# Optimization experiments

Measured on AMD Instinct MI355X. Metric: run time of the kernel, lower is better.

The kernel has to match this reference:

```python
import jax, jax.numpy as jnp
import numpy as np

B, T, TRAIN = 4, 2048, 1536
D, H, L, FF, V = 512, 8, 12, 2048, 100
DH = D // H
ROPE_BASE = 100000.0


def layer_norm(x, g, b, eps=1e-5):
    mu = jnp.mean(x, axis=-1, keepdims=True)
    var = jnp.mean(jnp.square(x - mu), axis=-1, keepdims=True)
    return (x - mu) * jax.lax.rsqrt(var + eps) * g + b


def rope_cos_sin(t, dh):
    inv_freq = 1.0 / (ROPE_BASE ** (jnp.arange(0, dh, 2, dtype=jnp.float32) / dh))  # (dh/2,)
    ang = jnp.arange(t, dtype=jnp.float32)[:, None] * inv_freq[None, :]  # (T, dh/2)
    return jnp.cos(ang), jnp.sin(ang)


def apply_rope_interleaved(x, cos, sin):
    # x: (B, T, H, DH); interleaved pairs (x0,x1),(x2,x3),...
    x1, x2 = x[..., 0::2], x[..., 1::2]
    c, s = cos[None, :, None, :], sin[None, :, None, :]
    r1 = x1 * c - x2 * s
    r2 = x1 * s + x2 * c
    return jnp.stack([r1, r2], axis=-1).reshape(x.shape)


def setup_inputs() -> dict:
    key = jax.random.key(0)
    ks = jax.random.split(key, 20)
    sc = 0.02
    inp = {
        'R': jax.random.normal(ks[0], (B, T, D), jnp.float32),
        'y_train': jax.random.randint(ks[1], (B, TRAIN), 0, V),
        'emb': jax.random.normal(ks[2], (V, D), jnp.float32) * sc,
        'Wqkv': jax.random.normal(ks[3], (L, D, 3 * D), jnp.float32) * sc,
        'bqkv': jnp.zeros((L, 3 * D), jnp.float32),
        'Wo': jax.random.normal(ks[4], (L, D, D), jnp.float32) * sc,
        'bo': jnp.zeros((L, D), jnp.float32),
        'ln1_g': jnp.ones((L, D), jnp.float32),
        'ln1_b': jnp.zeros((L, D), jnp.float32),
        'ln2_g': jnp.ones((L, D), jnp.float32),
        'ln2_b': jnp.zeros((L, D), jnp.float32),
        'W1': jax.random.normal(ks[5], (L, D, FF), jnp.float32) * sc,
        'b1': jnp.zeros((L, FF), jnp.float32),
        'W2': jax.random.normal(ks[6], (L, FF, D), jnp.float32) * sc,
        'b2': jnp.zeros((L, D), jnp.float32),
        'pW1': jax.random.normal(ks[7], (D, 2 * D), jnp.float32) * sc,
        'pb1': jnp.zeros((2 * D,), jnp.float32),
        'pW2': jax.random.normal(ks[8], (2 * D, V), jnp.float32) * sc,
        'pb2': jnp.zeros((V,), jnp.float32),
    }
    return inp


def icl_forward(R, y_train, emb, Wqkv, bqkv, Wo, bo, ln1_g, ln1_b, ln2_g, ln2_b, W1, b1, W2, b2, pW1, pb1, pW2, pb2):
    b, t, d = R.shape
    train = y_train.shape[1]
    # label embedding: train rows get emb[y], test rows get zeros
    y_emb = jnp.concatenate([emb[y_train], jnp.zeros((b, t - train, d), R.dtype)], axis=1)
    rep = R + y_emb
    # ICL mask: column j visible iff j < train or j == i
    idx = jnp.arange(t)
    allowed = (idx[None, :] < train) | (idx[:, None] == idx[None, :])
    mask = jnp.where(allowed, 0.0, -jnp.inf).astype(R.dtype)  # (T, T)
    cos, sin = rope_cos_sin(t, DH)
    scale = 1.0 / jnp.sqrt(jnp.asarray(DH, R.dtype))

    def block(x, p):
        wqkv, bq, wo, bob, g1, be1, g2, be2, w1, bb1, w2, bb2 = p
        h = layer_norm(x, g1, be1)
        qkv = h @ wqkv + bq  # (B,T,3D)
        q, k, v = jnp.split(qkv, 3, axis=-1)
        q = q.reshape(b, t, H, DH)
        k = k.reshape(b, t, H, DH)
        v = v.reshape(b, t, H, DH)
        q = apply_rope_interleaved(q, cos, sin)
        k = apply_rope_interleaved(k, cos, sin)
        scores = jnp.einsum('bthd,bshd->bhts', q, k) * scale + mask
        attn = jax.nn.softmax(scores, axis=-1)
        o = jnp.einsum('bhts,bshd->bthd', attn, v).reshape(b, t, d)
        x = x + o @ wo + bob
        h2 = layer_norm(x, g2, be2)
        x = x + jax.nn.gelu(h2 @ w1 + bb1) @ w2 + bb2
        return x, None

    rep, _ = jax.lax.scan(block, rep, (Wqkv, bqkv, Wo, bo, ln1_g, ln1_b, ln2_g, ln2_b, W1, b1, W2, b2))
    test = rep[:, train:, :]
    logits = jax.nn.gelu(test @ pW1 + pb1) @ pW2 + pb2  # (B, test, V)
    return logits


def reference(R, y_train, emb, Wqkv, bqkv, Wo, bo, ln1_g, ln1_b, ln2_g, ln2_b, W1, b1, W2, b2, pW1, pb1, pW2, pb2):
    return icl_forward(R, y_train, emb, Wqkv, bqkv, Wo, bo, ln1_g, ln1_b, ln2_g, ln2_b, W1, b1, W2, b2, pW1, pb1, pW2, pb2)
```

## Files before the change

kernel.cpp:

```cpp
#include <hip/hip_runtime.h>
#include <hip/hip_bf16.h>

#define BB 4
#define TT 2048
#define TRAIN 1536
#define DD 512
#define HH 8
#define LL 12
#define FFD 2048
#define VV 100
#define DH 64
#define NT (BB*TT)
#define NTEST (BB*(TT-TRAIN))

typedef __bf16 bf16x8 __attribute__((ext_vector_type(8)));
typedef float  f32x4  __attribute__((ext_vector_type(4)));
typedef unsigned int u32x4 __attribute__((ext_vector_type(4)));

#define GLDS16(g, l) __builtin_amdgcn_global_load_lds( \
    (const __attribute__((address_space(1))) void*)(g), \
    (__attribute__((address_space(3))) void*)(l), 16, 0, 0)

__global__ __launch_bounds__(256) void emb_add(const float* __restrict__ R,
                                               const int* __restrict__ y,
                                               const float* __restrict__ emb,
                                               float* __restrict__ rep) {
    int idx = blockIdx.x * 256 + threadIdx.x;
    int d = idx & 511;
    int n = idx >> 9;
    int t = n & (TT - 1);
    int b = n >> 11;
    float val = R[idx];
    if (t < TRAIN) {
        int tok = y[b * TRAIN + t];
        val += emb[(size_t)tok * DD + d];
    }
    rep[idx] = val;
}

__global__ __launch_bounds__(256) void ln_wave(const float* __restrict__ x,
                                               const float* __restrict__ g,
                                               const float* __restrict__ bta,
                                               __bf16* __restrict__ out) {
    int row = blockIdx.x * 4 + (threadIdx.x >> 6);
    int lane = threadIdx.x & 63;
    const float* xr = x + (size_t)row * DD + lane * 8;
    float4 a = *(const float4*)xr;
    float4 c = *(const float4*)(xr + 4);
    float s  = a.x + a.y + a.z + a.w + c.x + c.y + c.z + c.w;
    float sq = a.x*a.x + a.y*a.y + a.z*a.z + a.w*a.w + c.x*c.x + c.y*c.y + c.z*c.z + c.w*c.w;
#pragma unroll
    for (int off = 1; off < 64; off <<= 1) {
        s  += __shfl_xor(s, off);
        sq += __shfl_xor(sq, off);
    }
    float mu  = s * (1.0f / DD);
    float var = sq * (1.0f / DD) - mu * mu;
    float inv = rsqrtf(var + 1e-5f);
    const float* gp = g + lane * 8;
    const float* bp = bta + lane * 8;
    float4 g0 = *(const float4*)gp, g1 = *(const float4*)(gp + 4);
    float4 b0 = *(const float4*)bp, b1 = *(const float4*)(bp + 4);
    __bf16 o8[8];
    o8[0] = (__bf16)((a.x - mu) * inv * g0.x + b0.x);
    o8[1] = (__bf16)((a.y - mu) * inv * g0.y + b0.y);
    o8[2] = (__bf16)((a.z - mu) * inv * g0.z + b0.z);
    o8[3] = (__bf16)((a.w - mu) * inv * g0.w + b0.w);
    o8[4] = (__bf16)((c.x - mu) * inv * g1.x + b1.x);
    o8[5] = (__bf16)((c.y - mu) * inv * g1.y + b1.y);
    o8[6] = (__bf16)((c.z - mu) * inv * g1.z + b1.z);
    o8[7] = (__bf16)((c.w - mu) * inv * g1.w + b1.w);
    *(uint4*)(out + (size_t)row * DD + lane * 8) = *(uint4*)o8;
}

__global__ __launch_bounds__(256) void rope_tab(float* __restrict__ ctab, float* __restrict__ stab) {
    int idx = blockIdx.x * 256 + threadIdx.x;
    int p = idx & 31, t = idx >> 5;
    double freq = exp(-((double)(2 * p) / 64.0) * log(100000.0));
    double ang = (double)t * freq;
    ctab[idx] = (float)cos(ang);
    stab[idx] = (float)sin(ang);
}

#define QSCALE 0.1803368801111244f
__global__ __launch_bounds__(256) void rope_vt(const __bf16* __restrict__ qkv,
                                               const float* __restrict__ ctab,
                                               const float* __restrict__ stab,
                                               __bf16* __restrict__ qo,
                                               __bf16* __restrict__ ko,
                                               __bf16* __restrict__ vt) {
    int bh = blockIdx.y; int b = bh >> 3, h = bh & 7;
    int t0 = blockIdx.x * 64;
    __shared__ __bf16 tile[64][72];
    int tid = threadIdx.x;
    {
        int r = tid >> 2, cg = (tid & 3) * 16;
        const __bf16* src = qkv + (size_t)(b * TT + t0 + r) * (3 * DD) + 2 * DD + h * DH + cg;
        *(uint4*)&tile[r][cg]     = *(const uint4*)&src[0];
        *(uint4*)&tile[r][cg + 8] = *(const uint4*)&src[8];
    }
#pragma unroll
    for (int c = 0; c < 2; ++c) {
        int lin = c * 256 + tid;
        int tl = lin >> 3, u = lin & 7;
        int t = t0 + tl;
        const __bf16* base = qkv + (size_t)(b * TT + t) * (3 * DD) + h * DH + u * 8;
        uint4 qu = *(const uint4*)base;
        uint4 ku = *(const uint4*)(base + DD);
        float4 cv = *(const float4*)(ctab + t * 32 + u * 4);
        float4 sv = *(const float4*)(stab + t * 32 + u * 4);
        const __bf16* qp = (const __bf16*)&qu;
        const __bf16* kp = (const __bf16*)&ku;
        float cc[4] = {cv.x, cv.y, cv.z, cv.w};
        float ss[4] = {sv.x, sv.y, sv.z, sv.w};
        __bf16 oq[8], ok8[8];
#pragma unroll
        for (int j = 0; j < 4; ++j) {
            float x1 = (float)qp[2 * j], x2 = (float)qp[2 * j + 1];
            float k1 = (float)kp[2 * j], k2 = (float)kp[2 * j + 1];
            oq[2 * j]     = (__bf16)((x1 * cc[j] - x2 * ss[j]) * QSCALE);
            oq[2 * j + 1] = (__bf16)((x1 * ss[j] + x2 * cc[j]) * QSCALE);
            ok8[2 * j]     = (__bf16)(k1 * cc[j] - k2 * ss[j]);
            ok8[2 * j + 1] = (__bf16)(k1 * ss[j] + k2 * cc[j]);
        }
        size_t ob = ((size_t)bh * TT + t) * DH + u * 8;
        *(uint4*)(qo + ob) = *(uint4*)oq;
        *(uint4*)(ko + ob) = *(uint4*)ok8;
    }
    __syncthreads();
    {
        int dh = tid >> 2, tg = (tid & 3) * 16;
        __bf16 outv[16];
#pragma unroll
        for (int j = 0; j < 16; ++j) outv[j] = tile[tg + j][dh];
        __bf16* dst = vt + ((size_t)bh * DH + dh) * TT + t0 + tg;
        *(uint4*)&dst[0] = *(uint4*)&outv[0];
        *(uint4*)&dst[8] = *(uint4*)&outv[8];
    }
}

#define NCH (TRAIN/128)
#define EXP2(d, s) asm("v_exp_f32 %0, %1" : "=v"(d) : "v"(s))

__global__ __launch_bounds__(256, 2) void attn_mfma(const __bf16* __restrict__ q,
                                                    const __bf16* __restrict__ k,
                                                    const __bf16* __restrict__ vt,
                                                    __bf16* __restrict__ obuf) {
    __shared__ __align__(16) __bf16 Kb[2][128 * 64];
    __shared__ __align__(16) __bf16 Vb[2][64 * 128];
    __shared__ float sself[128];

    const int tid = threadIdx.x;
    const int lin = blockIdx.x;
    const int xcd = lin & 7, sblk = lin >> 3;
    const int bh = xcd * 4 + (sblk & 3);
    const int t0q = (sblk >> 2) * 128;
    const int b = bh >> 3, hh = bh & 7;
    const size_t kbase = (size_t)bh * TT * DH;
    const int w = tid >> 6;
    const int lane = tid & 63;
    const int l16 = lane & 15;
    const int quad = lane >> 4;
    const int x7 = l16 & 7;

    bf16x8 qa[2][2];
#pragma unroll
    for (int mi = 0; mi < 2; ++mi)
#pragma unroll
        for (int ks = 0; ks < 2; ++ks) {
            const __bf16* qg = q + kbase + (size_t)(t0q + w * 32 + mi * 16 + l16) * DH + ks * 32 + quad * 8;
            qa[mi][ks] = *(const bf16x8*)qg;
        }

    const int krl = lane >> 3, ksl = lane & 7;
    const int vrl = lane >> 4, vsl = lane & 15;

    f32x4 oa[2][4] = {};
    float lsum[2] = {0.f, 0.f};

    {
#pragma unroll
        for (int c = 0; c < 4; ++c) {
            int rb = w * 4 + c;
            GLDS16(k + kbase + (size_t)(rb * 8 + krl) * DH + ((ksl ^ krl) * 8), &Kb[0][rb * 512]);
            int dh = rb * 4 + vrl;
            GLDS16(vt + kbase + (size_t)dh * TT + ((vsl ^ (dh & 7)) * 8), &Vb[0][rb * 512]);
        }
    }

    for (int ci = 0; ci < NCH; ++ci) {
        __syncthreads();
        if (ci + 1 < NCH) {
            const __bf16* gk = k + kbase + (size_t)((ci + 1) * 128) * DH;
            __bf16* dK = Kb[(ci + 1) & 1];
            __bf16* dV = Vb[(ci + 1) & 1];
#pragma unroll
            for (int c = 0; c < 4; ++c) {
                int rb = w * 4 + c;
                GLDS16(gk + (size_t)(rb * 8 + krl) * DH + ((ksl ^ krl) * 8), dK + rb * 512);
                int dh = rb * 4 + vrl;
                GLDS16(vt + kbase + (size_t)dh * TT + (ci + 1) * 128 + ((vsl ^ (dh & 7)) * 8), dV + rb * 512);
            }
        }

        const __bf16* kc = Kb[ci & 1];
        f32x4 acc[2][8] = {};
        __builtin_amdgcn_s_setprio(1);
#pragma unroll
        for (int ks = 0; ks < 2; ++ks) {
            bf16x8 kf[8];
#pragma unroll
            for (int ni = 0; ni < 8; ++ni)
                kf[ni] = *(const bf16x8*)&kc[(ni * 16 + l16) * 64 + (((ks * 4 + quad) ^ x7) * 8)];
#pragma unroll
            for (int ni = 0; ni < 8; ++ni) {
                acc[0][ni] = __builtin_amdgcn_mfma_f32_16x16x32_bf16(kf[ni], qa[0][ks], acc[0][ni], 0, 0, 0);
                acc[1][ni] = __builtin_amdgcn_mfma_f32_16x16x32_bf16(kf[ni], qa[1][ks], acc[1][ni], 0, 0, 0);
            }
        }
        __builtin_amdgcn_s_setprio(0);

        u32x4 pa[2][4];
#pragma unroll
        for (int mi = 0; mi < 2; ++mi) {
            unsigned int pk[8][2];
            float rs = 0.f;
#pragma unroll
            for (int ni = 0; ni < 8; ++ni) {
                float p0, p1, p2, p3;
                EXP2(p0, acc[mi][ni][0]);
                EXP2(p1, acc[mi][ni][1]);
                EXP2(p2, acc[mi][ni][2]);
                EXP2(p3, acc[mi][ni][3]);
                rs += (p0 + p1) + (p2 + p3);
                asm("v_cvt_pk_bf16_f32 %0, %1, %2" : "=v"(pk[ni][0]) : "v"(p0), "v"(p1));
                asm("v_cvt_pk_bf16_f32 %0, %1, %2" : "=v"(pk[ni][1]) : "v"(p2), "v"(p3));
            }
            rs += __shfl_xor(rs, 16);
            rs += __shfl_xor(rs, 32);
            lsum[mi] += rs;
#pragma unroll
            for (int ks = 0; ks < 4; ++ks)
#pragma unroll
                for (int rr = 0; rr < 2; ++rr) {
                    unsigned int A = pk[2 * ks][rr], Bv = pk[2 * ks + 1][rr];
                    asm("v_permlane32_swap_b32 %0, %1" : "+v"(A), "+v"(Bv));
                    asm("v_permlane16_swap_b32 %0, %1" : "+v"(A), "+v"(Bv));
                    pa[mi][ks][rr]     = A;
                    pa[mi][ks][rr + 2] = Bv;
                }
        }

        const __bf16* vc = Vb[ci & 1];
        __builtin_amdgcn_s_setprio(1);
#pragma unroll
        for (int ks = 0; ks < 4; ++ks) {
            bf16x8 vf[4];
#pragma unroll
            for (int ni = 0; ni < 4; ++ni)
                vf[ni] = *(const bf16x8*)&vc[(ni * 16 + l16) * 128 + (((ks * 4 + quad) ^ x7) * 8)];
            bf16x8 pa0, pa1;
            { u32x4 t = pa[0][ks]; __builtin_memcpy(&pa0, &t, 16); }
            { u32x4 t = pa[1][ks]; __builtin_memcpy(&pa1, &t, 16); }
#pragma unroll
            for (int ni = 0; ni < 4; ++ni) {
                oa[0][ni] = __builtin_amdgcn_mfma_f32_16x16x32_bf16(pa0, vf[ni], oa[0][ni], 0, 0, 0);
                oa[1][ni] = __builtin_amdgcn_mfma_f32_16x16x32_bf16(pa1, vf[ni], oa[1][ni], 0, 0, 0);
            }
        }
        __builtin_amdgcn_s_setprio(0);
    }

    float lr[2][4];
#pragma unroll
    for (int mi = 0; mi < 2; ++mi)
#pragma unroll
        for (int r = 0; r < 4; ++r)
            lr[mi][r] = __shfl(lsum[mi], quad * 4 + r);

    if (t0q >= TRAIN) {
        __syncthreads();
        {
            int dh = tid >> 2, cg = (tid & 3) * 32;
            const __bf16* vg = vt + kbase + (size_t)dh * TT + t0q + cg;
#pragma unroll
            for (int u = 0; u < 4; ++u)
                *(uint4*)&Vb[0][dh * 128 + cg + u * 8] = *(const uint4*)&vg[u * 8];
            int row = tid >> 1, hf = tid & 1;
            const __bf16* qp = q + kbase + (size_t)(t0q + row) * DH + hf * 32;
            const __bf16* kp = k + kbase + (size_t)(t0q + row) * DH + hf * 32;
            float dacc = 0.f;
#pragma unroll
            for (int u = 0; u < 4; ++u) {
                uint4 uq = *(const uint4*)&qp[u * 8];
                uint4 uk = *(const uint4*)&kp[u * 8];
                const __bf16* pq = (const __bf16*)&uq;
                const __bf16* pk2 = (const __bf16*)&uk;
#pragma unroll
                for (int j = 0; j < 8; ++j) dacc += (float)pq[j] * (float)pk2[j];
            }
            dacc += __shfl_xor(dacc, 1);
            sself[row] = dacc;
        }
        __syncthreads();
#pragma unroll
        for (int mi = 0; mi < 2; ++mi)
#pragma unroll
            for (int r = 0; r < 4; ++r) {
                int qr = w * 32 + mi * 16 + quad * 4 + r;
                float pp;
                EXP2(pp, sself[qr]);
                lr[mi][r] += pp;
#pragma unroll
                for (int ni = 0; ni < 4; ++ni)
                    oa[mi][ni][r] += pp * (float)Vb[0][(ni * 16 + l16) * 128 + qr];
            }
    }

#pragma unroll
    for (int mi = 0; mi < 2; ++mi)
#pragma unroll
        for (int r = 0; r < 4; ++r) {
            float inv = 1.f / lr[mi][r];
            int trow = t0q + w * 32 + mi * 16 + quad * 4 + r;
            __bf16* op = obuf + ((size_t)(b * TT) + trow) * DD + hh * 64;
#pragma unroll
            for (int ni = 0; ni < 4; ++ni)
                op[ni * 16 + l16] = (__bf16)(oa[mi][ni][r] * inv);
        }
}

__global__ __launch_bounds__(256) void transpose_pad(const float* __restrict__ src,
                                                     __bf16* __restrict__ dst,
                                                     int K, int N) {
    __shared__ __bf16 t[32][33];
    int n0 = blockIdx.x * 32, k0 = blockIdx.y * 32;
    int tx = threadIdx.x & 31, ty = threadIdx.x >> 5;
#pragma unroll
    for (int i = 0; i < 4; ++i) {
        int nn = n0 + tx;
        t[ty + i * 8][tx] = (nn < N) ? (__bf16)src[(size_t)(k0 + ty + i * 8) * N + nn] : (__bf16)0.f;
    }
    __syncthreads();
#pragma unroll
    for (int i = 0; i < 4; ++i) {
        dst[(size_t)(n0 + ty + i * 8) * K + k0 + tx] = t[tx][ty + i * 8];
    }
}

__global__ __launch_bounds__(256) void transpose_all(const float* __restrict__ s0,
                                                     const float* __restrict__ s1,
                                                     const float* __restrict__ s2,
                                                     const float* __restrict__ s3,
                                                     __bf16* __restrict__ d0, __bf16* __restrict__ d1,
                                                     __bf16* __restrict__ d2, __bf16* __restrict__ d3) {
    int i = blockIdx.x;
    const float* src; __bf16* dst; int K, N, tx, ty;
    if (i < 768)       { src = s0; dst = d0; K = 512;  N = 1536; int j = i;        tx = j % 48; ty = j / 48; }
    else if (i < 1024) { src = s1; dst = d1; K = 512;  N = 512;  int j = i - 768;  tx = j % 16; ty = j / 16; }
    else if (i < 2048) { src = s2; dst = d2; K = 512;  N = 2048; int j = i - 1024; tx = j % 64; ty = j / 64; }
    else               { src = s3; dst = d3; K = 2048; N = 512;  int j = i - 2048; tx = j % 16; ty = j / 16; }
    __shared__ __bf16 t[32][33];
    int n0 = tx * 32, k0 = ty * 32;
    int lx = threadIdx.x & 31, ly = threadIdx.x >> 5;
#pragma unroll
    for (int c = 0; c < 4; ++c)
        t[ly + c * 8][lx] = (__bf16)src[(size_t)(k0 + ly + c * 8) * N + n0 + lx];
    __syncthreads();
#pragma unroll
    for (int c = 0; c < 4; ++c)
        dst[(size_t)(n0 + ly + c * 8) * K + k0 + lx] = t[lx][ly + c * 8];
}

template <int EP, int TN>
__global__ __launch_bounds__(256) void gemm_bt(const __bf16* __restrict__ A,
                                               const __bf16* __restrict__ Bt,
                                               const float* __restrict__ bias,
                                               float* __restrict__ resid,
                                               __bf16* __restrict__ Cout,
                                               int M, int N, int K) {
    constexpr int NI = TN / 32;
    __shared__ __align__(16) __bf16 As[2][128 * 32];
    __shared__ __align__(16) __bf16 Bs[2][TN * 32];
    const int tid = threadIdx.x;
    const int gx = gridDim.x;
    const int linb = blockIdx.x + gx * blockIdx.y;
    const int xs = gx >> 3;
    const int xcd = linb & 7, sb = linb >> 3;
    const int bx = xcd * xs + (sb % xs);
    const int by = sb / xs;
    const int m0 = bx * 128;
    const int n0 = by * TN;
    const int lane = tid & 63;
    const int w = tid >> 6;
    const int wm = (w >> 1) * 64, wn = (w & 1) * (TN / 2);
    const int lrow = lane & 15;
    const int kq = (lane >> 4) * 8;

    f32x4 acc[4][NI] = {};

    const int srA = w * 32 + (lane >> 2);
    const int srB = w * (TN / 4) + (lane >> 2);
    const int scol = (lane & 3) * 8;
    const __bf16* gA = A  + (size_t)(m0 + srA) * K + scol;
    const __bf16* gB = Bt + (size_t)(n0 + srB) * K + scol;
    __bf16* lA0 = &As[0][(w * 32) * 32];
    __bf16* lA0b = lA0 + 16 * 32;
    __bf16* lA1 = &As[1][(w * 32) * 32];
    __bf16* lA1b = lA1 + 16 * 32;
    __bf16* lB0 = &Bs[0][(w * (TN / 4)) * 32];
    __bf16* lB1 = &Bs[1][(w * (TN / 4)) * 32];

    const int nk = K >> 6;
    for (int kt = 0; kt < nk; ++kt) {
        const int k0 = kt << 6;
        GLDS16(gA + k0,            lA0);
        GLDS16(gA + 16 * K + k0,   lA0b);
        GLDS16(gA + k0 + 32,       lA1);
        GLDS16(gA + 16 * K + k0 + 32, lA1b);
        GLDS16(gB + k0,            lB0);
        GLDS16(gB + k0 + 32,       lB1);
        if constexpr (TN == 128) {
            GLDS16(gB + 16 * K + k0,      lB0 + 16 * 32);
            GLDS16(gB + 16 * K + k0 + 32, lB1 + 16 * 32);
        }
        __syncthreads();
#pragma unroll
        for (int ps = 0; ps < 2; ++ps) {
            bf16x8 afr[4], bfr[NI];
#pragma unroll
            for (int i = 0; i < 4; ++i)
                afr[i] = *(const bf16x8*)&As[ps][(wm + i * 16 + lrow) * 32 + kq];
#pragma unroll
            for (int i = 0; i < NI; ++i)
                bfr[i] = *(const bf16x8*)&Bs[ps][(wn + i * 16 + lrow) * 32 + kq];
#pragma unroll
            for (int mi = 0; mi < 4; ++mi)
#pragma unroll
                for (int ni = 0; ni < NI; ++ni)
                    acc[mi][ni] = __builtin_amdgcn_mfma_f32_16x16x32_bf16(afr[mi], bfr[ni], acc[mi][ni], 0, 0, 0);
        }
        __syncthreads();
    }

    const int crow = (lane >> 4) * 4;
    const int ccol = lane & 15;
#pragma unroll
    for (int mi = 0; mi < 4; ++mi) {
#pragma unroll
        for (int ni = 0; ni < NI; ++ni) {
            int gn = n0 + wn + ni * 16 + ccol;
            float bv = bias[gn];
#pragma unroll
            for (int r = 0; r < 4; ++r) {
                int gm = m0 + wm + mi * 16 + crow + r;
                float vvv = acc[mi][ni][r] + bv;
                if constexpr (EP == 1) {
                    float x = vvv;
                    vvv = x / (1.f + __expf(-1.5957691216f * (x + 0.044715f * x * x * x)));
                }
                if constexpr (EP == 2) {
                    resid[(size_t)gm * N + gn] += vvv;
                } else if constexpr (EP == 4) {
                    if (gn < VV) resid[(size_t)gm * VV + gn] = vvv;
                } else {
                    Cout[(size_t)gm * N + gn] = (__bf16)vvv;
                }
            }
        }
    }
}

__global__ __launch_bounds__(256) void cast_test(const float* __restrict__ rep, __bf16* __restrict__ testb) {
    int idx = blockIdx.x * 256 + threadIdx.x;
    int d = idx & 511;
    int i = idx >> 9;
    int ttk = i & 511;
    int b = i >> 9;
    testb[idx] = (__bf16)rep[(size_t)(b * TT + TRAIN + ttk) * DD + d];
}

__global__ void pad_bias(const float* __restrict__ pb2, float* __restrict__ pb2p) {
    int t = threadIdx.x;
    if (t < 128) pb2p[t] = (t < VV) ? pb2[t] : 0.f;
}

extern "C" void kernel_launch(void* const* d_in, const int* in_sizes, int n_in,
                              void* d_out, int out_size, void* d_ws, size_t ws_size,
                              hipStream_t stream) {
    const float* R    = (const float*)d_in[0];
    const int*   y    = (const int*)d_in[1];
    const float* emb  = (const float*)d_in[2];
    const float* Wqkv = (const float*)d_in[3];
    const float* bqkv = (const float*)d_in[4];
    const float* Wo   = (const float*)d_in[5];
    const float* bo   = (const float*)d_in[6];
    const float* ln1g = (const float*)d_in[7];
    const float* ln1b = (const float*)d_in[8];
    const float* ln2g = (const float*)d_in[9];
    const float* ln2b = (const float*)d_in[10];
    const float* W1   = (const float*)d_in[11];
    const float* b1   = (const float*)d_in[12];
    const float* W2   = (const float*)d_in[13];
    const float* b2   = (const float*)d_in[14];
    const float* pW1  = (const float*)d_in[15];
    const float* pb1  = (const float*)d_in[16];
    const float* pW2  = (const float*)d_in[17];
    const float* pb2  = (const float*)d_in[18];

    char* p = (char*)d_ws;
    float* rep    = (float*)p;  p += (size_t)NT * DD * 4;
    __bf16* hbuf  = (__bf16*)p; p += (size_t)NT * DD * 2;
    __bf16* qkv   = (__bf16*)p;
    __bf16* ffb   = qkv;        p += (size_t)NT * FFD * 2;
    __bf16* qb    = (__bf16*)p; p += (size_t)NT * DD * 2;
    __bf16* kb    = (__bf16*)p; p += (size_t)NT * DD * 2;
    __bf16* vtb   = (__bf16*)p; p += (size_t)NT * DD * 2;
    __bf16* obuf  = (__bf16*)p; p += (size_t)NT * DD * 2;
    __bf16* wqkvT = (__bf16*)p; p += (size_t)1536 * 512 * 2;
    __bf16* woT   = (__bf16*)p; p += (size_t)512 * 512 * 2;
    __bf16* w1T   = (__bf16*)p; p += (size_t)2048 * 512 * 2;
    __bf16* w2T   = (__bf16*)p; p += (size_t)512 * 2048 * 2;
    float* ctab   = (float*)p;  p += (size_t)TT * 32 * 4;
    float* stab   = (float*)p;  p += (size_t)TT * 32 * 4;
    float* pb2p   = (float*)p;  p += 512;
    __bf16* testb = hbuf;
    __bf16* hb    = obuf;

    emb_add<<<NT * DD / 256, 256, 0, stream>>>(R, y, emb, rep);
    rope_tab<<<TT * 32 / 256, 256, 0, stream>>>(ctab, stab);

    for (int l = 0; l < LL; ++l) {
        ln_wave<<<NT / 4, 256, 0, stream>>>(rep, ln1g + l * DD, ln1b + l * DD, hbuf);
        transpose_all<<<3072, 256, 0, stream>>>(Wqkv + (size_t)l * DD * 3 * DD, Wo + (size_t)l * DD * DD,
                                                W1 + (size_t)l * DD * FFD, W2 + (size_t)l * FFD * DD,
                                                wqkvT, woT, w1T, w2T);
        gemm_bt<0, 128><<<dim3(NT / 128, 1536 / 128), 256, 0, stream>>>(hbuf, wqkvT, bqkv + l * 3 * DD, nullptr, qkv, NT, 3 * DD, DD);
        rope_vt<<<dim3(TT / 64, BB * HH), 256, 0, stream>>>(qkv, ctab, stab, qb, kb, vtb);
        attn_mfma<<<dim3(512), 256, 0, stream>>>(qb, kb, vtb, obuf);
        gemm_bt<2, 64><<<dim3(NT / 128, 512 / 64), 256, 0, stream>>>(obuf, woT, bo + l * DD, rep, nullptr, NT, DD, DD);
        ln_wave<<<NT / 4, 256, 0, stream>>>(rep, ln2g + l * DD, ln2b + l * DD, hbuf);
        gemm_bt<1, 128><<<dim3(NT / 128, FFD / 128), 256, 0, stream>>>(hbuf, w1T, b1 + l * FFD, nullptr, ffb, NT, FFD, DD);
        gemm_bt<2, 64><<<dim3(NT / 128, 512 / 64), 256, 0, stream>>>(ffb, w2T, b2 + l * DD, rep, nullptr, NT, DD, FFD);
    }

    cast_test<<<NTEST * DD / 256, 256, 0, stream>>>(rep, testb);
    transpose_pad<<<dim3(1024 / 32, 512 / 32), 256, 0, stream>>>(pW1, w1T, DD, 2 * DD);
    gemm_bt<1, 64><<<dim3(NTEST / 128, 1024 / 64), 256, 0, stream>>>(testb, w1T, pb1, nullptr, hb, NTEST, 2 * DD, DD);
    pad_bias<<<1, 128, 0, stream>>>(pb2, pb2p);
    transpose_pad<<<dim3(128 / 32, 1024 / 32), 256, 0, stream>>>(pW2, w2T, 2 * DD, VV);
    gemm_bt<4, 128><<<dim3(NTEST / 128, 1), 256, 0, stream>>>(hb, w2T, pb2p, (float*)d_out, nullptr, NTEST, 128, 2 * DD);
}
```

Baseline: 2.296 ms.

## Fuse RoPE and V-transpose into QKV GEMM epilogue; hoist weight transposes

Adds a GEMM epilogue mode that applies bias, RoPE (via shuffle-xor pair exchange and a packed cos/sin table) and the Q scale directly when writing Q/K, and transposes V through shared memory into the V^T layout. This removes the separate rope_vt kernel and the round trip of the qkv intermediate through global memory. Separately, all twelve layers' weights are transposed and cast in one upfront launch when workspace allows, instead of one transpose launch per layer. The extra epilogue work and scattered per-element stores may slow the QKV GEMM somewhat, and the upfront transpose needs a larger workspace.

```diff
diff --git a/kernel.cpp b/kernel.cpp
--- a/kernel.cpp
+++ b/kernel.cpp
@@ -20,6 +20,8 @@
 #define GLDS16(g, l) __builtin_amdgcn_global_load_lds( \
     (const __attribute__((address_space(1))) void*)(g), \
     (__attribute__((address_space(3))) void*)(l), 16, 0, 0)
+
+#define QSCALE 0.1803368801111244f
 
 __global__ __launch_bounds__(256) void emb_add(const float* __restrict__ R,
                                                const int* __restrict__ y,
@@ -73,70 +75,12 @@
     *(uint4*)(out + (size_t)row * DD + lane * 8) = *(uint4*)o8;
 }
 
-__global__ __launch_bounds__(256) void rope_tab(float* __restrict__ ctab, float* __restrict__ stab) {
+__global__ __launch_bounds__(256) void cs_tab(float2* __restrict__ cs) {
     int idx = blockIdx.x * 256 + threadIdx.x;
     int p = idx & 31, t = idx >> 5;
     double freq = exp(-((double)(2 * p) / 64.0) * log(100000.0));
     double ang = (double)t * freq;
-    ctab[idx] = (float)cos(ang);
-    stab[idx] = (float)sin(ang);
-}
-
-#define QSCALE 0.1803368801111244f
-__global__ __launch_bounds__(256) void rope_vt(const __bf16* __restrict__ qkv,
-                                               const float* __restrict__ ctab,
-                                               const float* __restrict__ stab,
-                                               __bf16* __restrict__ qo,
-                                               __bf16* __restrict__ ko,
-                                               __bf16* __restrict__ vt) {
-    int bh = blockIdx.y; int b = bh >> 3, h = bh & 7;
-    int t0 = blockIdx.x * 64;
-    __shared__ __bf16 tile[64][72];
-    int tid = threadIdx.x;
-    {
-        int r = tid >> 2, cg = (tid & 3) * 16;
-        const __bf16* src = qkv + (size_t)(b * TT + t0 + r) * (3 * DD) + 2 * DD + h * DH + cg;
-        *(uint4*)&tile[r][cg]     = *(const uint4*)&src[0];
-        *(uint4*)&tile[r][cg + 8] = *(const uint4*)&src[8];
-    }
-#pragma unroll
-    for (int c = 0; c < 2; ++c) {
-        int lin = c * 256 + tid;
-        int tl = lin >> 3, u = lin & 7;
-        int t = t0 + tl;
-        const __bf16* base = qkv + (size_t)(b * TT + t) * (3 * DD) + h * DH + u * 8;
-        uint4 qu = *(const uint4*)base;
-        uint4 ku = *(const uint4*)(base + DD);
-        float4 cv = *(const float4*)(ctab + t * 32 + u * 4);
-        float4 sv = *(const float4*)(stab + t * 32 + u * 4);
-        const __bf16* qp = (const __bf16*)&qu;
-        const __bf16* kp = (const __bf16*)&ku;
-        float cc[4] = {cv.x, cv.y, cv.z, cv.w};
-        float ss[4] = {sv.x, sv.y, sv.z, sv.w};
-        __bf16 oq[8], ok8[8];
-#pragma unroll
-        for (int j = 0; j < 4; ++j) {
-            float x1 = (float)qp[2 * j], x2 = (float)qp[2 * j + 1];
-            float k1 = (float)kp[2 * j], k2 = (float)kp[2 * j + 1];
-            oq[2 * j]     = (__bf16)((x1 * cc[j] - x2 * ss[j]) * QSCALE);
-            oq[2 * j + 1] = (__bf16)((x1 * ss[j] + x2 * cc[j]) * QSCALE);
-            ok8[2 * j]     = (__bf16)(k1 * cc[j] - k2 * ss[j]);
-            ok8[2 * j + 1] = (__bf16)(k1 * ss[j] + k2 * cc[j]);
-        }
-        size_t ob = ((size_t)bh * TT + t) * DH + u * 8;
-        *(uint4*)(qo + ob) = *(uint4*)oq;
-        *(uint4*)(ko + ob) = *(uint4*)ok8;
-    }
-    __syncthreads();
-    {
-        int dh = tid >> 2, tg = (tid & 3) * 16;
-        __bf16 outv[16];
-#pragma unroll
-        for (int j = 0; j < 16; ++j) outv[j] = tile[tg + j][dh];
-        __bf16* dst = vt + ((size_t)bh * DH + dh) * TT + t0 + tg;
-        *(uint4*)&dst[0] = *(uint4*)&outv[0];
-        *(uint4*)&dst[8] = *(uint4*)&outv[8];
-    }
+    cs[idx] = make_float2((float)cos(ang), (float)sin(ang));
 }
 
 #define NCH (TRAIN/128)
@@ -355,6 +299,11 @@
                                                      __bf16* __restrict__ d0, __bf16* __restrict__ d1,
                                                      __bf16* __restrict__ d2, __bf16* __restrict__ d3) {
     int i = blockIdx.x;
+    int l = i / 3072; i -= l * 3072;
+    s0 += (size_t)l * 512 * 1536;  d0 += (size_t)l * 1536 * 512;
+    s1 += (size_t)l * 512 * 512;   d1 += (size_t)l * 512 * 512;
+    s2 += (size_t)l * 512 * 2048;  d2 += (size_t)l * 2048 * 512;
+    s3 += (size_t)l * 2048 * 512;  d3 += (size_t)l * 512 * 2048;
     const float* src; __bf16* dst; int K, N, tx, ty;
     if (i < 768)       { src = s0; dst = d0; K = 512;  N = 1536; int j = i;        tx = j % 48; ty = j / 48; }
     else if (i < 1024) { src = s1; dst = d1; K = 512;  N = 512;  int j = i - 768;  tx = j % 16; ty = j / 16; }
@@ -380,8 +329,9 @@
                                                __bf16* __restrict__ Cout,
                                                int M, int N, int K) {
     constexpr int NI = TN / 32;
-    __shared__ __align__(16) __bf16 As[2][128 * 32];
-    __shared__ __align__(16) __bf16 Bs[2][TN * 32];
+    __shared__ __align__(16) __bf16 smem[2 * 128 * 32 + 2 * TN * 32];
+    __bf16* const AsP[2] = { smem, smem + 4096 };
+    __bf16* const BsP[2] = { smem + 8192, smem + 8192 + TN * 32 };
     const int tid = threadIdx.x;
     const int gx = gridDim.x;
     const int linb = blockIdx.x + gx * blockIdx.y;
@@ -404,12 +354,12 @@
     const int scol = (lane & 3) * 8;
     const __bf16* gA = A  + (size_t)(m0 + srA) * K + scol;
     const __bf16* gB = Bt + (size_t)(n0 + srB) * K + scol;
-    __bf16* lA0 = &As[0][(w * 32) * 32];
+    __bf16* lA0 = &AsP[0][(w * 32) * 32];
     __bf16* lA0b = lA0 + 16 * 32;
-    __bf16* lA1 = &As[1][(w * 32) * 32];
+    __bf16* lA1 = &AsP[1][(w * 32) * 32];
     __bf16* lA1b = lA1 + 16 * 32;
-    __bf16* lB0 = &Bs[0][(w * (TN / 4)) * 32];
-    __bf16* lB1 = &Bs[1][(w * (TN / 4)) * 32];
+    __bf16* lB0 = &BsP[0][(w * (TN / 4)) * 32];
+    __bf16* lB1 = &BsP[1][(w * (TN / 4)) * 32];
 
     const int nk = K >> 6;
     for (int kt = 0; kt < nk; ++kt) {
@@ -430,10 +380,10 @@
             bf16x8 afr[4], bfr[NI];
 #pragma unroll
             for (int i = 0; i < 4; ++i)
-                afr[i] = *(const bf16x8*)&As[ps][(wm + i * 16 + lrow) * 32 + kq];
+                afr[i] = *(const bf16x8*)&AsP[ps][(wm + i * 16 + lrow) * 32 + kq];
 #pragma unroll
             for (int i = 0; i < NI; ++i)
-                bfr[i] = *(const bf16x8*)&Bs[ps][(wn + i * 16 + lrow) * 32 + kq];
+                bfr[i] = *(const bf16x8*)&BsP[ps][(wn + i * 16 + lrow) * 32 + kq];
 #pragma unroll
             for (int mi = 0; mi < 4; ++mi)
 #pragma unroll
@@ -445,6 +395,63 @@
 
     const int crow = (lane >> 4) * 4;
     const int ccol = lane & 15;
+
+    if constexpr (EP == 3) {
+        const int type = n0 >> 9;
+        if (type < 2) {
+            const float2* cs = (const float2*)resid;
+            __bf16* base = Cout + (size_t)type * NT * DD;
+#pragma unroll
+            for (int mi = 0; mi < 4; ++mi)
+#pragma unroll
+                for (int ni = 0; ni < NI; ++ni) {
+                    int gn = n0 + wn + ni * 16 + ccol;
+                    int col = gn & 511;
+                    int h = col >> 6, dh = col & 63, pp = dh >> 1;
+                    float bv = bias[gn];
+#pragma unroll
+                    for (int r = 0; r < 4; ++r) {
+                        int gm = m0 + wm + mi * 16 + crow + r;
+                        int t = gm & (TT - 1), bb = gm >> 11;
+                        float val = acc[mi][ni][r] + bv;
+                        float other = __shfl_xor(val, 1);
+                        float2 csv = cs[t * 32 + pp];
+                        float res = (dh & 1) ? (other * csv.y + val * csv.x)
+                                             : (val * csv.x - other * csv.y);
+                        if (type == 0) res *= QSCALE;
+                        base[((size_t)(bb * 8 + h) * TT + t) * DH + dh] = (__bf16)res;
+                    }
+                }
+        } else {
+            __syncthreads();
+            __bf16* lt = smem + w * 4096;
+#pragma unroll
+            for (int mi = 0; mi < 4; ++mi)
+#pragma unroll
+                for (int ni = 0; ni < NI; ++ni) {
+                    int lc = ni * 16 + ccol;
+                    float bv = bias[n0 + wn + ni * 16 + ccol];
+#pragma unroll
+                    for (int r = 0; r < 4; ++r) {
+                        int lr = mi * 16 + crow + r;
+                        lt[lc * 64 + lr] = (__bf16)(acc[mi][ni][r] + bv);
+                    }
+                }
+            __syncthreads();
+            int col0 = (n0 & 511) + wn;
+            int h = col0 >> 6;
+            int gmB = m0 + wm;
+            int bb = gmB >> 11, tbase = gmB & (TT - 1);
+            __bf16* vrow = Cout + (size_t)2 * NT * DD + ((size_t)((bb * 8 + h) * 64) + lane) * TT + tbase;
+#pragma unroll
+            for (int u = 0; u < 8; ++u) {
+                bf16x8 vv = *(const bf16x8*)&lt[lane * 64 + u * 8];
+                *(uint4*)&vrow[u * 8] = *(uint4*)&vv;
+            }
+        }
+        return;
+    }
+
 #pragma unroll
     for (int mi = 0; mi < 4; ++mi) {
 #pragma unroll
@@ -511,37 +518,48 @@
     char* p = (char*)d_ws;
     float* rep    = (float*)p;  p += (size_t)NT * DD * 4;
     __bf16* hbuf  = (__bf16*)p; p += (size_t)NT * DD * 2;
-    __bf16* qkv   = (__bf16*)p;
-    __bf16* ffb   = qkv;        p += (size_t)NT * FFD * 2;
+    __bf16* ffb   = (__bf16*)p; p += (size_t)NT * FFD * 2;
     __bf16* qb    = (__bf16*)p; p += (size_t)NT * DD * 2;
     __bf16* kb    = (__bf16*)p; p += (size_t)NT * DD * 2;
     __bf16* vtb   = (__bf16*)p; p += (size_t)NT * DD * 2;
     __bf16* obuf  = (__bf16*)p; p += (size_t)NT * DD * 2;
-    __bf16* wqkvT = (__bf16*)p; p += (size_t)1536 * 512 * 2;
-    __bf16* woT   = (__bf16*)p; p += (size_t)512 * 512 * 2;
-    __bf16* w1T   = (__bf16*)p; p += (size_t)2048 * 512 * 2;
-    __bf16* w2T   = (__bf16*)p; p += (size_t)512 * 2048 * 2;
-    float* ctab   = (float*)p;  p += (size_t)TT * 32 * 4;
-    float* stab   = (float*)p;  p += (size_t)TT * 32 * 4;
+    float2* cstab = (float2*)p; p += (size_t)TT * 32 * 8;
     float* pb2p   = (float*)p;  p += 512;
+    const size_t perl_qkv = (size_t)1536 * 512, perl_wo = (size_t)512 * 512;
+    const size_t perl_w1  = (size_t)2048 * 512, perl_w2 = (size_t)512 * 2048;
+    const size_t perl_bytes = (perl_qkv + perl_wo + perl_w1 + perl_w2) * 2;
+    size_t used = (size_t)(p - (char*)d_ws);
+    bool big = (ws_size > used) && ((ws_size - used) >= 12 * perl_bytes);
+    int nl = big ? 12 : 1;
+    __bf16* wqkvT = (__bf16*)p; p += perl_qkv * 2 * nl;
+    __bf16* woT   = (__bf16*)p; p += perl_wo * 2 * nl;
+    __bf16* w1T   = (__bf16*)p; p += perl_w1 * 2 * nl;
+    __bf16* w2T   = (__bf16*)p; p += perl_w2 * 2 * nl;
     __bf16* testb = hbuf;
     __bf16* hb    = obuf;
 
     emb_add<<<NT * DD / 256, 256, 0, stream>>>(R, y, emb, rep);
-    rope_tab<<<TT * 32 / 256, 256, 0, stream>>>(ctab, stab);
+    cs_tab<<<TT * 32 / 256, 256, 0, stream>>>(cstab);
+    if (big)
+        transpose_all<<<3072 * 12, 256, 0, stream>>>(Wqkv, Wo, W1, W2, wqkvT, woT, w1T, w2T);
 
     for (int l = 0; l < LL; ++l) {
         ln_wave<<<NT / 4, 256, 0, stream>>>(rep, ln1g + l * DD, ln1b + l * DD, hbuf);
-        transpose_all<<<3072, 256, 0, stream>>>(Wqkv + (size_t)l * DD * 3 * DD, Wo + (size_t)l * DD * DD,
-                                                W1 + (size_t)l * DD * FFD, W2 + (size_t)l * FFD * DD,
-                                                wqkvT, woT, w1T, w2T);
-        gemm_bt<0, 128><<<dim3(NT / 128, 1536 / 128), 256, 0, stream>>>(hbuf, wqkvT, bqkv + l * 3 * DD, nullptr, qkv, NT, 3 * DD, DD);
-        rope_vt<<<dim3(TT / 64, BB * HH), 256, 0, stream>>>(qkv, ctab, stab, qb, kb, vtb);
+        if (!big)
+            transpose_all<<<3072, 256, 0, stream>>>(Wqkv + (size_t)l * DD * 3 * DD, Wo + (size_t)l * DD * DD,
+                                                    W1 + (size_t)l * DD * FFD, W2 + (size_t)l * FFD * DD,
+                                                    wqkvT, woT, w1T, w2T);
+        __bf16* wq = wqkvT + (big ? (size_t)l * perl_qkv : 0);
+        __bf16* wo2 = woT  + (big ? (size_t)l * perl_wo  : 0);
+        __bf16* w12 = w1T  + (big ? (size_t)l * perl_w1  : 0);
+        __bf16* w22 = w2T  + (big ? (size_t)l * perl_w2  : 0);
+        gemm_bt<3, 128><<<dim3(NT / 128, 1536 / 128), 256, 0, stream>>>(hbuf, wq, bqkv + l * 3 * DD,
+                                                                        (float*)cstab, qb, NT, 3 * DD, DD);
         attn_mfma<<<dim3(512), 256, 0, stream>>>(qb, kb, vtb, obuf);
-        gemm_bt<2, 64><<<dim3(NT / 128, 512 / 64), 256, 0, stream>>>(obuf, woT, bo + l * DD, rep, nullptr, NT, DD, DD);
+        gemm_bt<2, 64><<<dim3(NT / 128, 512 / 64), 256, 0, stream>>>(obuf, wo2, bo + l * DD, rep, nullptr, NT, DD, DD);
         ln_wave<<<NT / 4, 256, 0, stream>>>(rep, ln2g + l * DD, ln2b + l * DD, hbuf);
-        gemm_bt<1, 128><<<dim3(NT / 128, FFD / 128), 256, 0, stream>>>(hbuf, w1T, b1 + l * FFD, nullptr, ffb, NT, FFD, DD);
-        gemm_bt<2, 64><<<dim3(NT / 128, 512 / 64), 256, 0, stream>>>(ffb, w2T, b2 + l * DD, rep, nullptr, NT, DD, FFD);
+        gemm_bt<1, 128><<<dim3(NT / 128, FFD / 128), 256, 0, stream>>>(hbuf, w12, b1 + l * FFD, nullptr, ffb, NT, FFD, DD);
+        gemm_bt<2, 64><<<dim3(NT / 128, 512 / 64), 256, 0, stream>>>(ffb, w22, b2 + l * DD, rep, nullptr, NT, DD, FFD);
     }
 
     cast_test<<<NTEST * DD / 256, 256, 0, stream>>>(rep, testb);
```

Result: no change. 2.299 ms (+0.2%).
